# Optimization experiments

Measured on AMD Instinct MI355X. Metric: run time of the kernel, lower is better.

## Reference

```python
import jax, jax.numpy as jnp
import numpy as np

EMBED_DIM = 1024
NUM_HEADS = 16
HEAD_DIM = EMBED_DIM // NUM_HEADS
MLP_HIDDEN = 4096
B, S = 2, 2048


def setup_inputs() -> dict:
    key = jax.random.key(0)
    ks = jax.random.split(key, 10)
    sd = lambda fan_in: 1.0 / np.sqrt(fan_in)
    x = jax.random.normal(ks[0], (B, S, EMBED_DIM), dtype=jnp.float32)
    # weights stored (in, out) so y = x @ W + b (same math as torch Linear)
    w_qkv = jax.random.normal(ks[1], (EMBED_DIM, 3 * EMBED_DIM), jnp.float32) * sd(EMBED_DIM)
    w_proj = jax.random.normal(ks[2], (EMBED_DIM, EMBED_DIM), jnp.float32) * sd(EMBED_DIM)
    b_proj = jnp.zeros((EMBED_DIM,), jnp.float32)
    w_fc1 = jax.random.normal(ks[3], (EMBED_DIM, MLP_HIDDEN), jnp.float32) * sd(EMBED_DIM)
    b_fc1 = jnp.zeros((MLP_HIDDEN,), jnp.float32)
    w_fc2 = jax.random.normal(ks[4], (MLP_HIDDEN, EMBED_DIM), jnp.float32) * sd(MLP_HIDDEN)
    b_fc2 = jnp.zeros((EMBED_DIM,), jnp.float32)
    g1 = jnp.ones((EMBED_DIM,), jnp.float32)
    be1 = jnp.zeros((EMBED_DIM,), jnp.float32)
    g2 = jnp.ones((EMBED_DIM,), jnp.float32)
    be2 = jnp.zeros((EMBED_DIM,), jnp.float32)
    return {"x": x, "w_qkv": w_qkv, "w_proj": w_proj, "b_proj": b_proj,
            "w_fc1": w_fc1, "b_fc1": b_fc1, "w_fc2": w_fc2, "b_fc2": b_fc2,
            "g1": g1, "be1": be1, "g2": g2, "be2": be2}


def _layernorm(x, g, b, eps=1e-5):
    mu = jnp.mean(x, axis=-1, keepdims=True)
    var = jnp.var(x, axis=-1, keepdims=True)
    return (x - mu) * jax.lax.rsqrt(var + eps) * g + b


def _block(x, w_qkv, w_proj, b_proj, w_fc1, b_fc1, w_fc2, b_fc2, g1, be1, g2, be2):
    # --- attention branch ---
    h = _layernorm(x, g1, be1)
    qkv = h @ w_qkv  # [B,S,3D]
    qkv = qkv.reshape(B, S, 3, NUM_HEADS, HEAD_DIM).transpose(2, 0, 3, 1, 4)
    q, k, v = qkv[0], qkv[1], qkv[2]  # each [B,H,S,Dh]
    scale = 1.0 / np.sqrt(HEAD_DIM).astype(np.float32)
    dots = jnp.einsum('bhqd,bhkd->bhqk', q, k) * scale  # naive full score matrix
    attn = jax.nn.softmax(dots, axis=-1)
    out = jnp.einsum('bhqk,bhkd->bhqd', attn, v)
    out = out.transpose(0, 2, 1, 3).reshape(B, S, EMBED_DIM)
    x = x + (out @ w_proj + b_proj)
    # --- mlp branch ---
    h2 = _layernorm(x, g2, be2)
    mlp = jax.nn.gelu(h2 @ w_fc1 + b_fc1, approximate=False) @ w_fc2 + b_fc2
    return x + mlp


def reference(x, w_qkv, w_proj, b_proj, w_fc1, b_fc1, w_fc2, b_fc2, g1, be1, g2, be2):
    return _block(x, w_qkv, w_proj, b_proj, w_fc1, b_fc1, w_fc2, b_fc2, g1, be1, g2, be2)
```

## Files before the change

### kernel.cpp

```cpp
#include <hip/hip_runtime.h>

typedef __attribute__((ext_vector_type(8))) short short8;
typedef __attribute__((ext_vector_type(4))) float f32x4;

#define MFMA16(a, b, c) __builtin_amdgcn_mfma_f32_16x16x32_bf16((a), (b), (c), 0, 0, 0)

static __device__ __forceinline__ unsigned short f2bf(float f) {
    unsigned int u = __float_as_uint(f);
    return (unsigned short)((u + 0x7fffu + ((u >> 16) & 1u)) >> 16);
}

static __device__ __forceinline__ void glds16(const unsigned short* g, unsigned short* l) {
    __builtin_amdgcn_global_load_lds(
        (const __attribute__((address_space(1))) unsigned int*)g,
        (__attribute__((address_space(3))) unsigned int*)l, 16, 0, 0);
}

__global__ __launch_bounds__(256) void convt_kernel(const float* __restrict__ W,
                                                    unsigned short* __restrict__ WT,
                                                    int K, int N) {
    __shared__ unsigned short Ts[32][33];
    int t = threadIdx.x;
    int bk = blockIdx.y * 32, bn = blockIdx.x * 32;
    int r = t >> 3, c = (t & 7) * 4;
    float4 w = *(const float4*)&W[(size_t)(bk + r) * N + bn + c];
    Ts[c + 0][r] = f2bf(w.x); Ts[c + 1][r] = f2bf(w.y);
    Ts[c + 2][r] = f2bf(w.z); Ts[c + 3][r] = f2bf(w.w);
    __syncthreads();
    ushort4 o;
    o.x = Ts[r][c]; o.y = Ts[r][c + 1]; o.z = Ts[r][c + 2]; o.w = Ts[r][c + 3];
    *(ushort4*)&WT[(size_t)(bn + r) * K + bk + c] = o;
}

__global__ __launch_bounds__(256) void ln_kernel(const float* __restrict__ x,
                                                 const float* __restrict__ g,
                                                 const float* __restrict__ be,
                                                 unsigned short* __restrict__ y) {
    int row = blockIdx.x;
    const float* xr = x + (size_t)row * 1024;
    unsigned short* yr = y + (size_t)row * 1024;
    int t = threadIdx.x;
    float v[4];
    float sum = 0.f, sq = 0.f;
#pragma unroll
    for (int i = 0; i < 4; ++i) {
        float f = xr[t + i * 256];
        v[i] = f; sum += f; sq += f * f;
    }
#pragma unroll
    for (int o = 32; o > 0; o >>= 1) { sum += __shfl_down(sum, o); sq += __shfl_down(sq, o); }
    __shared__ float red[8];
    int wave = t >> 6, lane = t & 63;
    if (lane == 0) { red[wave] = sum; red[4 + wave] = sq; }
    __syncthreads();
    sum = red[0] + red[1] + red[2] + red[3];
    sq  = red[4] + red[5] + red[6] + red[7];
    float mean = sum * (1.f / 1024.f);
    float var  = sq * (1.f / 1024.f) - mean * mean;
    float rstd = rsqrtf(var + 1e-5f);
#pragma unroll
    for (int i = 0; i < 4; ++i) {
        int c = t + i * 256;
        yr[c] = f2bf((v[i] - mean) * rstd * g[c] + be[c]);
    }
}

template <int BN>
__global__ __launch_bounds__(256) void gemm_kernel(const unsigned short* __restrict__ A,
                                                   const unsigned short* __restrict__ BT,
                                                   const float* __restrict__ bias,
                                                   const float* __restrict__ resid,
                                                   void* __restrict__ C,
                                                   int M, int N, int K, int act, int cF32) {
    constexpr int NT = BN / 32;
    __shared__ __align__(16) unsigned short As[128][32];
    __shared__ __align__(16) unsigned short Bs[BN][32];
    int t = threadIdx.x, wave = t >> 6, lane = t & 63;
    int lm = lane & 15, quad = lane >> 4, k8 = quad * 8;
    int wm = (wave >> 1) * 64, wn = (wave & 1) * (BN / 2);
    int br = blockIdx.y * 128, bc = blockIdx.x * BN;

    int srow = lane >> 2, scol = (lane & 3) * 8;
    const unsigned short* Ag0 = A + (size_t)(br + wave * 32 + srow) * K + scol;
    const unsigned short* Ag1 = Ag0 + (size_t)16 * K;
    unsigned short* Al0 = &As[wave * 32][0];
    unsigned short* Al1 = &As[wave * 32 + 16][0];
    const unsigned short* Bg0 = BT + (size_t)(bc + wave * (BN / 4) + srow) * K + scol;
    const unsigned short* Bg1 = Bg0 + (size_t)16 * K;
    unsigned short* Bl0 = &Bs[wave * (BN / 4)][0];
    unsigned short* Bl1 = &Bs[wave * (BN / 4) + 16][0];

    f32x4 zero4 = {0.f, 0.f, 0.f, 0.f};
    f32x4 acc[4][NT];
#pragma unroll
    for (int i = 0; i < 4; ++i)
#pragma unroll
        for (int j = 0; j < NT; ++j) acc[i][j] = zero4;

    for (int k0 = 0; k0 < K; k0 += 32) {
        __syncthreads();
        glds16(Ag0 + k0, Al0);
        glds16(Ag1 + k0, Al1);
        glds16(Bg0 + k0, Bl0);
        if (BN == 128) glds16(Bg1 + k0, Bl1);
        __syncthreads();
        short8 af[4], bf[NT];
#pragma unroll
        for (int i = 0; i < 4; ++i) af[i] = *(const short8*)&As[wm + i * 16 + lm][k8];
#pragma unroll
        for (int j = 0; j < NT; ++j) bf[j] = *(const short8*)&Bs[wn + j * 16 + lm][k8];
#pragma unroll
        for (int i = 0; i < 4; ++i)
#pragma unroll
            for (int j = 0; j < NT; ++j) acc[i][j] = MFMA16(af[i], bf[j], acc[i][j]);
    }

#pragma unroll
    for (int i = 0; i < 4; ++i)
#pragma unroll
        for (int j = 0; j < NT; ++j) {
            int col = bc + wn + j * 16 + lm;
            float bv = bias ? bias[col] : 0.f;
#pragma unroll
            for (int r = 0; r < 4; ++r) {
                int row = br + wm + i * 16 + quad * 4 + r;
                float v = acc[i][j][r] + bv;
                if (act == 1) v = 0.5f * v * (1.f + erff(v * 0.70710678118f));
                size_t idx = (size_t)row * N + col;
                if (resid) v += resid[idx];
                if (cF32) ((float*)C)[idx] = v;
                else ((unsigned short*)C)[idx] = f2bf(v);
            }
        }
}

__global__ __launch_bounds__(256) void attn_kernel(const unsigned short* __restrict__ qkv,
                                                   unsigned short* __restrict__ out) {
    __shared__ __align__(16) unsigned short Qs[64][72];
    __shared__ __align__(16) unsigned short Ks[64][72];
    __shared__ __align__(16) unsigned short Vs[64][72];
    __shared__ __align__(16) unsigned short Ps[4][16][72];

    int t = threadIdx.x, wave = t >> 6, lane = t & 63;
    int lm = lane & 15, quad = lane >> 4, k8 = quad * 8;
    int bh = blockIdx.y, b = bh >> 4, h = bh & 15;
    int q0 = blockIdx.x * 64;
    const unsigned short* base = qkv + (size_t)b * 2048 * 3072 + h * 64;
    const unsigned short* kb = base + 1024;
    const unsigned short* vb = base + 2048;

    {
        int r = t >> 2, c = (t & 3) * 16;
        const unsigned short* src = base + (size_t)(q0 + r) * 3072 + c;
        *(uint4*)&Qs[r][c] = *(const uint4*)src;
        *(uint4*)&Qs[r][c + 8] = *(const uint4*)(src + 8);
    }
    __syncthreads();
    short8 qa0 = *(const short8*)&Qs[wave * 16 + lm][k8];
    short8 qa1 = *(const short8*)&Qs[wave * 16 + lm][32 + k8];

    f32x4 zero4 = {0.f, 0.f, 0.f, 0.f};
    f32x4 oacc[4] = {zero4, zero4, zero4, zero4};
    float lsum[4] = {0.f, 0.f, 0.f, 0.f};

    int sr = t >> 2, sc = (t & 3) * 16;

    for (int kt = 0; kt < 2048; kt += 64) {
        __syncthreads();
        {
            const unsigned short* ksrc = kb + (size_t)(kt + sr) * 3072 + sc;
            *(uint4*)&Ks[sr][sc] = *(const uint4*)ksrc;
            *(uint4*)&Ks[sr][sc + 8] = *(const uint4*)(ksrc + 8);
            const unsigned short* vsrc = vb + (size_t)(kt + sr) * 3072 + sc;
            unsigned short tv[16] __attribute__((aligned(16)));
            *(uint4*)&tv[0] = *(const uint4*)vsrc;
            *(uint4*)&tv[8] = *(const uint4*)(vsrc + 8);
            int kg = sr >> 3, kw = sr & 7;
#pragma unroll
            for (int j = 0; j < 16; ++j) {
                int d = sc + j;
                Vs[d][((kg ^ ((d >> 3) & 7)) << 3) + kw] = tv[j];
            }
        }
        __syncthreads();

        f32x4 s[4];
#pragma unroll
        for (int nt = 0; nt < 4; ++nt) {
            short8 kf0 = *(const short8*)&Ks[nt * 16 + lm][k8];
            short8 kf1 = *(const short8*)&Ks[nt * 16 + lm][32 + k8];
            f32x4 a = zero4;
            a = MFMA16(qa0, kf0, a);
            a = MFMA16(qa1, kf1, a);
            s[nt] = a;
        }

#pragma unroll
        for (int r = 0; r < 4; ++r) {
            int row = quad * 4 + r;
            int sw = (row >> 1) & 7;
#pragma unroll
            for (int nt = 0; nt < 4; ++nt) {
                float p = __expf(s[nt][r] * 0.125f - 8.0f);
                lsum[r] += p;
                int g = (nt << 1) + (lm >> 3);
                Ps[wave][row][((g ^ sw) << 3) + (lm & 7)] = f2bf(p);
            }
        }

#pragma unroll
        for (int kh = 0; kh < 2; ++kh) {
            int pg = (kh << 2) + quad;
            short8 pa = *(const short8*)&Ps[wave][lm][(pg ^ ((lm >> 1) & 7)) << 3];
#pragma unroll
            for (int nt = 0; nt < 4; ++nt) {
                int d = nt * 16 + lm;
                short8 vf = *(const short8*)&Vs[d][(pg ^ ((d >> 3) & 7)) << 3];
                oacc[nt] = MFMA16(pa, vf, oacc[nt]);
            }
        }
    }

#pragma unroll
    for (int r = 0; r < 4; ++r) {
        float l = lsum[r];
        l += __shfl_xor(l, 1); l += __shfl_xor(l, 2);
        l += __shfl_xor(l, 4); l += __shfl_xor(l, 8);
        float inv = 1.f / l;
        int qrow = q0 + wave * 16 + quad * 4 + r;
        size_t o = ((size_t)(b * 2048 + qrow)) * 1024 + h * 64;
#pragma unroll
        for (int nt = 0; nt < 4; ++nt) out[o + nt * 16 + lm] = f2bf(oacc[nt][r] * inv);
    }
}

extern "C" void kernel_launch(void* const* d_in, const int* in_sizes, int n_in,
                              void* d_out, int out_size, void* d_ws, size_t ws_size,
                              hipStream_t stream) {
    const float* x      = (const float*)d_in[0];
    const float* w_qkv  = (const float*)d_in[1];
    const float* w_proj = (const float*)d_in[2];
    const float* b_proj = (const float*)d_in[3];
    const float* w_fc1  = (const float*)d_in[4];
    const float* b_fc1  = (const float*)d_in[5];
    const float* w_fc2  = (const float*)d_in[6];
    const float* b_fc2  = (const float*)d_in[7];
    const float* g1     = (const float*)d_in[8];
    const float* be1    = (const float*)d_in[9];
    const float* g2     = (const float*)d_in[10];
    const float* be2    = (const float*)d_in[11];
    float* out = (float*)d_out;
    unsigned short* sb = (unsigned short*)d_out;

    char* ws = (char*)d_ws;
    unsigned short* wqkvT  = (unsigned short*)ws;
    unsigned short* wprojT = (unsigned short*)(ws + ((size_t)6u << 20));
    unsigned short* wfc1T  = (unsigned short*)(ws + ((size_t)8u << 20));
    unsigned short* wfc2T  = (unsigned short*)(ws + ((size_t)16u << 20));
    unsigned short* qkv    = (unsigned short*)(ws + ((size_t)24u << 20));

    convt_kernel<<<dim3(96, 32),  dim3(256), 0, stream>>>(w_qkv,  wqkvT, 1024, 3072);
    convt_kernel<<<dim3(32, 32),  dim3(256), 0, stream>>>(w_proj, wprojT, 1024, 1024);
    convt_kernel<<<dim3(128, 32), dim3(256), 0, stream>>>(w_fc1,  wfc1T, 1024, 4096);
    convt_kernel<<<dim3(32, 128), dim3(256), 0, stream>>>(w_fc2,  wfc2T, 4096, 1024);
    ln_kernel<<<dim3(4096), dim3(256), 0, stream>>>(x, g1, be1, sb);
    gemm_kernel<128><<<dim3(24, 32), dim3(256), 0, stream>>>(
        sb, wqkvT, nullptr, nullptr, qkv, 4096, 3072, 1024, 0, 0);
    attn_kernel<<<dim3(32, 32), dim3(256), 0, stream>>>(qkv, sb);

    if (ws_size >= ((size_t)72u << 20)) {
        float*          x2 = (float*)(ws + ((size_t)24u << 20));
        unsigned short* m1 = (unsigned short*)(ws + ((size_t)40u << 20));
        gemm_kernel<64><<<dim3(16, 32), dim3(256), 0, stream>>>(
            sb, wprojT, b_proj, x, x2, 4096, 1024, 1024, 0, 1);
        ln_kernel<<<dim3(4096), dim3(256), 0, stream>>>(x2, g2, be2, sb);
        gemm_kernel<128><<<dim3(32, 32), dim3(256), 0, stream>>>(
            sb, wfc1T, b_fc1, nullptr, m1, 4096, 4096, 1024, 1, 0);
        gemm_kernel<64><<<dim3(16, 32), dim3(256), 0, stream>>>(
            m1, wfc2T, b_fc2, x2, out, 4096, 1024, 4096, 0, 1);
    } else {
        float*          x2  = (float*)(ws + ((size_t)24u << 20));
        unsigned short* m1c = (unsigned short*)(ws + ((size_t)40u << 20));
        unsigned short* h2  = (unsigned short*)d_out + ((size_t)4u << 20);
        gemm_kernel<64><<<dim3(16, 32), dim3(256), 0, stream>>>(
            sb, wprojT, b_proj, x, x2, 4096, 1024, 1024, 0, 1);
        ln_kernel<<<dim3(4096), dim3(256), 0, stream>>>(x2, g2, be2, h2);
        for (int c = 0; c < 4; ++c) {
            size_t ro = (size_t)c * 1024;
            gemm_kernel<128><<<dim3(32, 8), dim3(256), 0, stream>>>(
                h2 + ro * 1024, wfc1T, b_fc1, nullptr, m1c, 1024, 4096, 1024, 1, 0);
            gemm_kernel<64><<<dim3(16, 8), dim3(256), 0, stream>>>(
                m1c, wfc2T, b_fc2, x2 + ro * 1024, out + ro * 1024, 1024, 1024, 4096, 0, 1);
        }
    }
}
```

Measured before the change: 456.4 us.

## Pre-swizzle K and transpose V once, stream tiles via direct-to-LDS loads

Adds a prep kernel that writes K into a per-head contiguous swizzled layout and V into a pre-transposed, swizzled tile layout. A new attention kernel then loads each 64-key tile with global_load_lds DMA instead of per-thread strided loads and scalar scattered LDS transposes. This removes the V transpose that every query block repeated inside the attention loop, at the cost of one extra pass over K/V and more workspace. The four weight conversion launches are also merged into a single launch.

```diff
diff --git a/kernel.cpp b/kernel.cpp
--- a/kernel.cpp
+++ b/kernel.cpp
@@ -16,12 +16,20 @@
         (__attribute__((address_space(3))) unsigned int*)l, 16, 0, 0);
 }
 
-__global__ __launch_bounds__(256) void convt_kernel(const float* __restrict__ W,
-                                                    unsigned short* __restrict__ WT,
-                                                    int K, int N) {
+__global__ __launch_bounds__(256) void convt_all_kernel(
+    const float* __restrict__ w_qkv, const float* __restrict__ w_proj,
+    const float* __restrict__ w_fc1, const float* __restrict__ w_fc2,
+    unsigned short* __restrict__ wqkvT, unsigned short* __restrict__ wprojT,
+    unsigned short* __restrict__ wfc1T, unsigned short* __restrict__ wfc2T) {
     __shared__ unsigned short Ts[32][33];
+    int id = blockIdx.x;
+    const float* W; unsigned short* WT; int K, N, bx, by;
+    if (id < 3072)      { W = w_qkv;  WT = wqkvT;  K = 1024; N = 3072; bx = id % 96;  by = id / 96; }
+    else if (id < 4096) { id -= 3072; W = w_proj; WT = wprojT; K = 1024; N = 1024; bx = id & 31; by = id >> 5; }
+    else if (id < 8192) { id -= 4096; W = w_fc1;  WT = wfc1T;  K = 1024; N = 4096; bx = id & 127; by = id >> 7; }
+    else                { id -= 8192; W = w_fc2;  WT = wfc2T;  K = 4096; N = 1024; bx = id & 31; by = id >> 5; }
     int t = threadIdx.x;
-    int bk = blockIdx.y * 32, bn = blockIdx.x * 32;
+    int bk = by * 32, bn = bx * 32;
     int r = t >> 3, c = (t & 7) * 4;
     float4 w = *(const float4*)&W[(size_t)(bk + r) * N + bn + c];
     Ts[c + 0][r] = f2bf(w.x); Ts[c + 1][r] = f2bf(w.y);
@@ -134,13 +142,148 @@
         }
 }
 
+__global__ __launch_bounds__(256) void kvprep_kernel(const unsigned short* __restrict__ qkv,
+                                                     unsigned short* __restrict__ Kp,
+                                                     unsigned short* __restrict__ Vt) {
+    __shared__ unsigned short Vl[64][72];
+    int t = threadIdx.x;
+    int w = blockIdx.x, bh = blockIdx.y;
+    int b = bh >> 4, h = bh & 15;
+    int kt = w * 64;
+    int sl = t >> 2, c = (t & 3) * 16;
+    const unsigned short* src = qkv + (size_t)(b * 2048 + kt + sl) * 3072 + h * 64 + c;
+
+    {
+        uint4 k0 = *(const uint4*)(src + 1024);
+        uint4 k1 = *(const uint4*)(src + 1024 + 8);
+        int sw = sl & 7;
+        int o0 = (c >> 3), o1 = o0 + 1;
+        unsigned short* krow = Kp + ((size_t)bh * 2048 + kt + sl) * 64;
+        *(uint4*)&krow[(o0 ^ sw) << 3] = k0;
+        *(uint4*)&krow[(o1 ^ sw) << 3] = k1;
+    }
+    {
+        uint4 v0 = *(const uint4*)(src + 2048);
+        uint4 v1 = *(const uint4*)(src + 2048 + 8);
+        *(uint4*)&Vl[sl][c] = v0;
+        *(uint4*)&Vl[sl][c + 8] = v1;
+    }
+    __syncthreads();
+    {
+        int d = t >> 2, kc = (t & 3) * 16;
+        unsigned short vv[16];
+#pragma unroll
+        for (int i = 0; i < 16; ++i) vv[i] = Vl[kc + i][d];
+        int sw = d & 7;
+        int ko0 = kc >> 3, ko1 = ko0 + 1;
+        unsigned short* vrow = Vt + ((((size_t)bh * 32 + w) * 64) + d) * 64;
+        *(uint4*)&vrow[(ko0 ^ sw) << 3] = *(uint4*)&vv[0];
+        *(uint4*)&vrow[(ko1 ^ sw) << 3] = *(uint4*)&vv[8];
+    }
+}
+
+__global__ __launch_bounds__(256) void attn2_kernel(const unsigned short* __restrict__ qkv,
+                                                    const unsigned short* __restrict__ Kp,
+                                                    const unsigned short* __restrict__ Vt,
+                                                    unsigned short* __restrict__ out) {
+    __shared__ __align__(16) unsigned short Qs[64][72];
+    __shared__ __align__(16) unsigned short Ks[4096];
+    __shared__ __align__(16) unsigned short Vs[4096];
+    __shared__ __align__(16) unsigned short Ps[4][16][72];
+
+    int t = threadIdx.x, wave = t >> 6, lane = t & 63;
+    int lm = lane & 15, quad = lane >> 4, k8 = quad * 8;
+    int bh = blockIdx.y, b = bh >> 4, h = bh & 15;
+    int q0 = blockIdx.x * 64;
+    const unsigned short* base = qkv + (size_t)b * 2048 * 3072 + h * 64;
+
+    {
+        int r = t >> 2, c = (t & 3) * 16;
+        const unsigned short* src = base + (size_t)(q0 + r) * 3072 + c;
+        *(uint4*)&Qs[r][c] = *(const uint4*)src;
+        *(uint4*)&Qs[r][c + 8] = *(const uint4*)(src + 8);
+    }
+    __syncthreads();
+    short8 qa0 = *(const short8*)&Qs[wave * 16 + lm][k8];
+    short8 qa1 = *(const short8*)&Qs[wave * 16 + lm][32 + k8];
+
+    f32x4 zero4 = {0.f, 0.f, 0.f, 0.f};
+    f32x4 oacc[4] = {zero4, zero4, zero4, zero4};
+    float lsum[4] = {0.f, 0.f, 0.f, 0.f};
+
+    for (int kt = 0; kt < 2048; kt += 64) {
+        __syncthreads();
+        {
+            const unsigned short* kg = Kp + ((size_t)bh * 2048 + kt) * 64 + wave * 1024 + (lane << 3);
+            unsigned short* kl = &Ks[wave * 1024];
+            glds16(kg, kl);
+            glds16(kg + 512, kl + 512);
+            const unsigned short* vg = Vt + (((size_t)bh * 32 + (kt >> 6)) * 64) * 64 + wave * 1024 + (lane << 3);
+            unsigned short* vl = &Vs[wave * 1024];
+            glds16(vg, vl);
+            glds16(vg + 512, vl + 512);
+        }
+        __syncthreads();
+
+        f32x4 s[4];
+#pragma unroll
+        for (int nt = 0; nt < 4; ++nt) {
+            int key = nt * 16 + lm;
+            int swk = lm & 7;
+            const unsigned short* krow = &Ks[key * 64];
+            short8 kf0 = *(const short8*)&krow[(quad ^ swk) << 3];
+            short8 kf1 = *(const short8*)&krow[((quad ^ swk) ^ 4) << 3];
+            f32x4 a = zero4;
+            a = MFMA16(qa0, kf0, a);
+            a = MFMA16(qa1, kf1, a);
+            s[nt] = a;
+        }
+
+#pragma unroll
+        for (int r = 0; r < 4; ++r) {
+            int row = quad * 4 + r;
+            int sw = (row >> 1) & 7;
+#pragma unroll
+            for (int nt = 0; nt < 4; ++nt) {
+                float p = __expf(s[nt][r] * 0.125f - 8.0f);
+                lsum[r] += p;
+                int g = (nt << 1) + (lm >> 3);
+                Ps[wave][row][((g ^ sw) << 3) + (lm & 7)] = f2bf(p);
+            }
+        }
+
+#pragma unroll
+        for (int kh = 0; kh < 2; ++kh) {
+            int pg = (kh << 2) + quad;
+            short8 pa = *(const short8*)&Ps[wave][lm][(pg ^ ((lm >> 1) & 7)) << 3];
+#pragma unroll
+            for (int nt = 0; nt < 4; ++nt) {
+                int d = nt * 16 + lm;
+                short8 vf = *(const short8*)&Vs[d * 64 + ((pg ^ (lm & 7)) << 3)];
+                oacc[nt] = MFMA16(pa, vf, oacc[nt]);
+            }
+        }
+    }
+
+#pragma unroll
+    for (int r = 0; r < 4; ++r) {
+        float l = lsum[r];
+        l += __shfl_xor(l, 1); l += __shfl_xor(l, 2);
+        l += __shfl_xor(l, 4); l += __shfl_xor(l, 8);
+        float inv = 1.f / l;
+        int qrow = q0 + wave * 16 + quad * 4 + r;
+        size_t o = ((size_t)(b * 2048 + qrow)) * 1024 + h * 64;
+#pragma unroll
+        for (int nt = 0; nt < 4; ++nt) out[o + nt * 16 + lm] = f2bf(oacc[nt][r] * inv);
+    }
+}
+
 __global__ __launch_bounds__(256) void attn_kernel(const unsigned short* __restrict__ qkv,
                                                    unsigned short* __restrict__ out) {
     __shared__ __align__(16) unsigned short Qs[64][72];
     __shared__ __align__(16) unsigned short Ks[64][72];
     __shared__ __align__(16) unsigned short Vs[64][72];
     __shared__ __align__(16) unsigned short Ps[4][16][72];
-
     int t = threadIdx.x, wave = t >> 6, lane = t & 63;
     int lm = lane & 15, quad = lane >> 4, k8 = quad * 8;
     int bh = blockIdx.y, b = bh >> 4, h = bh & 15;
@@ -148,7 +291,6 @@
     const unsigned short* base = qkv + (size_t)b * 2048 * 3072 + h * 64;
     const unsigned short* kb = base + 1024;
     const unsigned short* vb = base + 2048;
-
     {
         int r = t >> 2, c = (t & 3) * 16;
         const unsigned short* src = base + (size_t)(q0 + r) * 3072 + c;
@@ -158,13 +300,10 @@
     __syncthreads();
     short8 qa0 = *(const short8*)&Qs[wave * 16 + lm][k8];
     short8 qa1 = *(const short8*)&Qs[wave * 16 + lm][32 + k8];
-
     f32x4 zero4 = {0.f, 0.f, 0.f, 0.f};
     f32x4 oacc[4] = {zero4, zero4, zero4, zero4};
     float lsum[4] = {0.f, 0.f, 0.f, 0.f};
-
     int sr = t >> 2, sc = (t & 3) * 16;
-
     for (int kt = 0; kt < 2048; kt += 64) {
         __syncthreads();
         {
@@ -183,7 +322,6 @@
             }
         }
         __syncthreads();
-
         f32x4 s[4];
 #pragma unroll
         for (int nt = 0; nt < 4; ++nt) {
@@ -194,7 +332,6 @@
             a = MFMA16(qa1, kf1, a);
             s[nt] = a;
         }
-
 #pragma unroll
         for (int r = 0; r < 4; ++r) {
             int row = quad * 4 + r;
@@ -207,7 +344,6 @@
                 Ps[wave][row][((g ^ sw) << 3) + (lm & 7)] = f2bf(p);
             }
         }
-
 #pragma unroll
         for (int kh = 0; kh < 2; ++kh) {
             int pg = (kh << 2) + quad;
@@ -220,7 +356,6 @@
             }
         }
     }
-
 #pragma unroll
     for (int r = 0; r < 4; ++r) {
         float l = lsum[r];
@@ -259,18 +394,19 @@
     unsigned short* wfc2T  = (unsigned short*)(ws + ((size_t)16u << 20));
     unsigned short* qkv    = (unsigned short*)(ws + ((size_t)24u << 20));
 
-    convt_kernel<<<dim3(96, 32),  dim3(256), 0, stream>>>(w_qkv,  wqkvT, 1024, 3072);
-    convt_kernel<<<dim3(32, 32),  dim3(256), 0, stream>>>(w_proj, wprojT, 1024, 1024);
-    convt_kernel<<<dim3(128, 32), dim3(256), 0, stream>>>(w_fc1,  wfc1T, 1024, 4096);
-    convt_kernel<<<dim3(32, 128), dim3(256), 0, stream>>>(w_fc2,  wfc2T, 4096, 1024);
+    convt_all_kernel<<<dim3(12288), dim3(256), 0, stream>>>(
+        w_qkv, w_proj, w_fc1, w_fc2, wqkvT, wprojT, wfc1T, wfc2T);
     ln_kernel<<<dim3(4096), dim3(256), 0, stream>>>(x, g1, be1, sb);
     gemm_kernel<128><<<dim3(24, 32), dim3(256), 0, stream>>>(
         sb, wqkvT, nullptr, nullptr, qkv, 4096, 3072, 1024, 0, 0);
-    attn_kernel<<<dim3(32, 32), dim3(256), 0, stream>>>(qkv, sb);
 
     if (ws_size >= ((size_t)72u << 20)) {
+        unsigned short* Kp = (unsigned short*)(ws + ((size_t)48u << 20));
+        unsigned short* Vt = (unsigned short*)(ws + ((size_t)56u << 20));
         float*          x2 = (float*)(ws + ((size_t)24u << 20));
         unsigned short* m1 = (unsigned short*)(ws + ((size_t)40u << 20));
+        kvprep_kernel<<<dim3(32, 32), dim3(256), 0, stream>>>(qkv, Kp, Vt);
+        attn2_kernel<<<dim3(32, 32), dim3(256), 0, stream>>>(qkv, Kp, Vt, sb);
         gemm_kernel<64><<<dim3(16, 32), dim3(256), 0, stream>>>(
             sb, wprojT, b_proj, x, x2, 4096, 1024, 1024, 0, 1);
         ln_kernel<<<dim3(4096), dim3(256), 0, stream>>>(x2, g2, be2, sb);
@@ -282,6 +418,7 @@
         float*          x2  = (float*)(ws + ((size_t)24u << 20));
         unsigned short* m1c = (unsigned short*)(ws + ((size_t)40u << 20));
         unsigned short* h2  = (unsigned short*)d_out + ((size_t)4u << 20);
+        attn_kernel<<<dim3(32, 32), dim3(256), 0, stream>>>(qkv, sb);
         gemm_kernel<64><<<dim3(16, 32), dim3(256), 0, stream>>>(
             sb, wprojT, b_proj, x, x2, 4096, 1024, 1024, 0, 1);
         ln_kernel<<<dim3(4096), dim3(256), 0, stream>>>(x2, g2, be2, h2);
```

Result: faster. 442.3 us (-3.1%).
